# Optimization experiments

Hardware: AMD Instinct MI355X
Metric: run time of the kernel (lower is better)

Reference implementation:

```python
import jax, jax.numpy as jnp
import numpy as np

N_NODES = 10000
N_EDGES = 320000
H = 256
L = 3
EPS = 1e-5


def _mlp2(x, w1, b1, w2, b2):
    # Linear -> ReLU -> Linear
    return jax.nn.relu(x @ w1 + b1) @ w2 + b2


def _layer_norm(x, g, b):
    mu = jnp.mean(x, axis=-1, keepdims=True)
    var = jnp.var(x, axis=-1, keepdims=True)
    return (x - mu) * jax.lax.rsqrt(var + EPS) * g + b


def setup_inputs() -> dict:
    key = jax.random.key(0)
    ks = jax.random.split(key, 24)
    s = 0.02
    inp = {
        "node_features": jax.random.normal(ks[0], (N_NODES, H), dtype=jnp.float32),
        "edge_index": jax.random.randint(ks[1], (2, N_EDGES), 0, N_NODES, dtype=jnp.int64),
        # node encoder (Linear 256->256, ReLU, Linear 256->256)
        "ne_w1": jax.random.normal(ks[2], (H, H), dtype=jnp.float32) * s,
        "ne_b1": jnp.zeros((H,), jnp.float32),
        "ne_w2": jax.random.normal(ks[3], (H, H), dtype=jnp.float32) * s,
        "ne_b2": jnp.zeros((H,), jnp.float32),
        # per-layer message MLP (2H->H, ReLU, H->H), stacked over L layers
        "msg_w1": jax.random.normal(ks[4], (L, 2 * H, H), dtype=jnp.float32) * s,
        "msg_b1": jnp.zeros((L, H), jnp.float32),
        "msg_w2": jax.random.normal(ks[5], (L, H, H), dtype=jnp.float32) * s,
        "msg_b2": jnp.zeros((L, H), jnp.float32),
        # per-layer update MLP (2H->H, ReLU, H->H)
        "upd_w1": jax.random.normal(ks[6], (L, 2 * H, H), dtype=jnp.float32) * s,
        "upd_b1": jnp.zeros((L, H), jnp.float32),
        "upd_w2": jax.random.normal(ks[7], (L, H, H), dtype=jnp.float32) * s,
        "upd_b2": jnp.zeros((L, H), jnp.float32),
        # per-layer LayerNorm
        "ln_g": jnp.ones((L, H), jnp.float32),
        "ln_b": jnp.zeros((L, H), jnp.float32),
        # readout MLP
        "ro_w1": jax.random.normal(ks[8], (H, H), dtype=jnp.float32) * s,
        "ro_b1": jnp.zeros((H,), jnp.float32),
        "ro_w2": jax.random.normal(ks[9], (H, H), dtype=jnp.float32) * s,
        "ro_b2": jnp.zeros((H,), jnp.float32),
    }
    return inp


def reference(node_features, edge_index, ne_w1, ne_b1, ne_w2, ne_b2,
              msg_w1, msg_b1, msg_w2, msg_b2,
              upd_w1, upd_b1, upd_w2, upd_b2,
              ln_g, ln_b, ro_w1, ro_b1, ro_w2, ro_b2):
    n_nodes = node_features.shape[0]
    src, dst = edge_index[0], edge_index[1]

    # node encoder
    x = _mlp2(node_features, ne_w1, ne_b1, ne_w2, ne_b2)  # [N, H]

    # message passing layers (edge_attr is unused in the original layer)
    for l in range(L):
        cat_e = jnp.concatenate([x[src], x[dst]], axis=-1)          # [E, 2H]
        messages = _mlp2(cat_e, msg_w1[l], msg_b1[l], msg_w2[l], msg_b2[l])  # [E, H]
        aggregated = jax.ops.segment_sum(messages, dst, num_segments=n_nodes)  # [N, H]
        cat_n = jnp.concatenate([x, aggregated], axis=-1)           # [N, 2H]
        updated = _mlp2(cat_n, upd_w1[l], upd_b1[l], upd_w2[l], upd_b2[l])
        x = _layer_norm(x + updated, ln_g[l], ln_b[l])

    # mean readout
    g = jnp.mean(x, axis=0)  # [H]
    return _mlp2(g, ro_w1, ro_b1, ro_w2, ro_b2)  # [H]
```

## Files before the change

### kernel.cpp

```cpp
#include <hip/hip_runtime.h>

#define NN 10000
#define NE 320000
#define HD 256
#define NL 3

typedef unsigned short ushort_t;
typedef __attribute__((ext_vector_type(8))) short bf16x8;
typedef __attribute__((ext_vector_type(4))) float f32x4;

#define MFMA __builtin_amdgcn_mfma_f32_16x16x32_bf16

#define WAITV(N) asm volatile("s_waitcnt vmcnt(" #N ")" ::: "memory")
#define SCHEDPIN() __builtin_amdgcn_sched_barrier(0)
#define LGKMBAR() do { asm volatile("s_waitcnt lgkmcnt(0)" ::: "memory"); \
                       __builtin_amdgcn_s_barrier(); __builtin_amdgcn_sched_barrier(0); } while (0)

__device__ __forceinline__ unsigned short f2bf(float x) {
    unsigned u = __float_as_uint(x);
    unsigned rounding = 0x7FFFu + ((u >> 16) & 1u);
    return (unsigned short)((u + rounding) >> 16);
}
__device__ __forceinline__ float bf2f(unsigned short u) {
    return __uint_as_float(((unsigned)u) << 16);
}
__device__ __forceinline__ bf16x8 cvt8(float4 lo, float4 hi) {
    bf16x8 r;
    r[0] = (short)f2bf(lo.x); r[1] = (short)f2bf(lo.y);
    r[2] = (short)f2bf(lo.z); r[3] = (short)f2bf(lo.w);
    r[4] = (short)f2bf(hi.x); r[5] = (short)f2bf(hi.y);
    r[6] = (short)f2bf(hi.z); r[7] = (short)f2bf(hi.w);
    return r;
}
__device__ __forceinline__ void dma16(const void* g, void* l) {
    __builtin_amdgcn_global_load_lds(
        (const __attribute__((address_space(1))) unsigned int*)g,
        (__attribute__((address_space(3))) unsigned int*)l, 16, 0, 0);
}


__global__ void hist_deg(const int* __restrict__ dst, int* __restrict__ deg, int E) {
    int e = blockIdx.x * blockDim.x + threadIdx.x;
    if (e < E) atomicAdd(&deg[dst[e]], 1);
}

__global__ __launch_bounds__(1024) void scan_csr(const int* __restrict__ deg,
                                                 int* __restrict__ row_start,
                                                 int* __restrict__ cursor,
                                                 float* __restrict__ degf,
                                                 float* __restrict__ gsum, int n) {
    __shared__ int wsum[16];
    __shared__ int carry_s;
    int tid = threadIdx.x, lane = tid & 63, wid = tid >> 6;
    if (tid < HD) gsum[tid] = 0.f;
    if (tid == 0) carry_s = 0;
    __syncthreads();
    for (int base = 0; base < n; base += 1024) {
        int i = base + tid;
        int v = (i < n) ? deg[i] : 0;
        int s = v;
        #pragma unroll
        for (int off = 1; off < 64; off <<= 1) {
            int t = __shfl_up(s, off);
            if (lane >= off) s += t;
        }
        if (lane == 63) wsum[wid] = s;
        __syncthreads();
        if (wid == 0 && lane < 16) {
            int ws = wsum[lane];
            #pragma unroll
            for (int off = 1; off < 16; off <<= 1) {
                int t = __shfl_up(ws, off);
                if (lane >= off) ws += t;
            }
            wsum[lane] = ws;
        }
        __syncthreads();
        int carry = carry_s;
        int wpre = (wid > 0) ? wsum[wid - 1] : 0;
        int incl = carry + wpre + s;
        int excl = incl - v;
        if (i < n) { row_start[i] = excl; cursor[i] = excl; degf[i] = (float)v; }
        __syncthreads();
        if (tid == 1023) carry_s = incl;
        __syncthreads();
    }
    if (tid == 0) row_start[n] = carry_s;
}

__global__ void scatter_src(const int* __restrict__ src, const int* __restrict__ dst,
                            int* __restrict__ cursor, int* __restrict__ src_sorted, int E) {
    int e = blockIdx.x * blockDim.x + threadIdx.x;
    if (e < E) {
        int pos = atomicAdd(&cursor[dst[e]], 1);
        src_sorted[pos] = src[e];
    }
}


struct TDesc { const float* src; ushort_t* dst; int transpose; };
struct TArgs { TDesc d[20]; };

__global__ __launch_bounds__(256) void conv_t(TArgs args) {
    __shared__ ushort_t tile[64][65];
    const float* src = args.d[blockIdx.y].src;
    ushort_t* dst = args.d[blockIdx.y].dst;
    int tr = args.d[blockIdx.y].transpose;
    int t = blockIdx.x;
    int r0 = (t >> 2) * 64, c0 = (t & 3) * 64;
    int tid = threadIdx.x;
    int rr = tid >> 4, cc4 = (tid & 15) * 4;
    if (!tr) {
        #pragma unroll
        for (int i = 0; i < 4; ++i) {
            int r = r0 + rr + i * 16;
            float4 v = *(const float4*)(src + (size_t)r * HD + c0 + cc4);
            ushort4 o = { f2bf(v.x), f2bf(v.y), f2bf(v.z), f2bf(v.w) };
            *(ushort4*)(dst + (size_t)r * HD + c0 + cc4) = o;
        }
        return;
    }
    #pragma unroll
    for (int i = 0; i < 4; ++i) {
        int r = rr + i * 16;
        float4 v = *(const float4*)(src + (size_t)(r0 + r) * HD + c0 + cc4);
        tile[cc4 + 0][r] = f2bf(v.x);
        tile[cc4 + 1][r] = f2bf(v.y);
        tile[cc4 + 2][r] = f2bf(v.z);
        tile[cc4 + 3][r] = f2bf(v.w);
    }
    __syncthreads();
    #pragma unroll
    for (int i = 0; i < 4; ++i) {
        int c = rr + i * 16;
        ushort4 o = { tile[c][cc4], tile[c][cc4 + 1], tile[c][cc4 + 2], tile[c][cc4 + 3] };
        *(ushort4*)(dst + (size_t)(c0 + c) * HD + r0 + cc4) = o;
    }
}

__global__ __launch_bounds__(256) void bias_compose(const float* __restrict__ mb2,
                                                    const float* __restrict__ uw1,
                                                    float* __restrict__ out) {
    int l = blockIdx.x, c = threadIdx.x;
    const float* b2l = mb2 + (size_t)l * HD;
    const float* u1b = uw1 + (size_t)l * 2 * HD * HD + (size_t)HD * HD;
    float s = 0.f;
    for (int k = 0; k < HD; ++k) s += b2l[k] * u1b[(size_t)k * HD + c];
    out[(size_t)l * HD + c] = s;
}

__global__ __launch_bounds__(256) void gemm_w2u(
    const ushort_t* __restrict__ Abase, const ushort_t* __restrict__ Btbase,
    ushort_t* __restrict__ outBase)
{
    const ushort_t* A  = Abase  + (size_t)blockIdx.z * HD * HD;
    const ushort_t* Bt = Btbase + (size_t)blockIdx.z * HD * HD;
    ushort_t* outB     = outBase + (size_t)blockIdx.z * HD * HD;
    int tid = threadIdx.x;
    int wid = tid >> 6, lane = tid & 63;
    int wm = wid >> 1, wn = wid & 1;
    int row0 = blockIdx.x * 64 + wm * 32;
    int col0 = blockIdx.y * 64 + wn * 32;
    int lm = lane & 15, lk = (lane >> 4) * 8;
    f32x4 acc[2][2] = {};
    const ushort_t* a0p = A + (size_t)(row0 + lm) * HD + lk;
    const ushort_t* a1p = A + (size_t)(row0 + 16 + lm) * HD + lk;
    const ushort_t* b0p = Bt + (size_t)(col0 + lm) * HD + lk;
    const ushort_t* b1p = Bt + (size_t)(col0 + 16 + lm) * HD + lk;
    #pragma unroll
    for (int k0 = 0; k0 < HD; k0 += 32) {
        bf16x8 a0 = *(const bf16x8*)(a0p + k0);
        bf16x8 a1 = *(const bf16x8*)(a1p + k0);
        bf16x8 b0 = *(const bf16x8*)(b0p + k0);
        bf16x8 b1 = *(const bf16x8*)(b1p + k0);
        acc[0][0] = MFMA(a0, b0, acc[0][0], 0, 0, 0);
        acc[0][1] = MFMA(a0, b1, acc[0][1], 0, 0, 0);
        acc[1][0] = MFMA(a1, b0, acc[1][0], 0, 0, 0);
        acc[1][1] = MFMA(a1, b1, acc[1][1], 0, 0, 0);
    }
    int orow = (lane >> 4) * 4;
    #pragma unroll
    for (int mi = 0; mi < 2; ++mi)
        #pragma unroll
        for (int r = 0; r < 4; ++r) {
            int row = row0 + mi * 16 + orow + r;
            #pragma unroll
            for (int ni = 0; ni < 2; ++ni) {
                int col = col0 + ni * 16 + lm;
                outB[(size_t)row * HD + col] = f2bf(acc[mi][ni][r]);
            }
        }
}

__device__ __forceinline__ int swz(int row, int byte_in_row) {
    return row * 512 + (byte_in_row ^ ((row & 7) << 4));
}


__global__ __launch_bounds__(512, 4) void enc_pq(
    const float* __restrict__ A, const ushort_t* __restrict__ B1t,
    const ushort_t* __restrict__ B2t,
    const float* __restrict__ b1, const float* __restrict__ b2,
    const ushort_t* __restrict__ Pw1t, const ushort_t* __restrict__ Pw1b,
    const float* __restrict__ pqb1,
    float* __restrict__ xF, ushort_t* __restrict__ xB,
    ushort_t* __restrict__ P, float* __restrict__ Q, int M)
{
    __shared__ char wlds[8][2][2][2048];
    __shared__ char hid[16 * 512];
    int tid = threadIdx.x;
    int w = tid >> 6, lane = tid & 63;
    int lm = lane & 15, q = lane >> 4;
    int row0 = blockIdx.x * 16;
    int col0 = w * 32;
    int cA = col0 + lm, cB = col0 + 16 + lm;

    auto stageW = [&](const ushort_t* Mt, int k0, int p, int m) {
        #pragma unroll
        for (int i = 0; i < 2; ++i) {
            int col = col0 + 16 * i + (lane >> 2);
            int qs = (lane & 3) ^ (col & 3) ^ ((col >> 2) & 3);
            dma16((const char*)Mt + (size_t)col * 512 + k0 * 2 + qs * 16,
                  wlds[w][p][m] + i * 1024);
        }
    };
    auto readB = [&](int p, int m, int ni) -> bf16x8 {
        int col = col0 + 16 * ni + lm;
        int q2 = q ^ (col & 3) ^ ((col >> 2) & 3);
        return *(const bf16x8*)(wlds[w][p][m] + ni * 1024 + lm * 64 + q2 * 16);
    };

    float b1v[2] = { b1[cA], b1[cB] };
    float b2v[2] = { b2[cA], b2[cB] };
    float pqv[2] = { pqb1[cA], pqb1[cB] };

    const float* ap = A + (size_t)(row0 + lm) * HD + q * 8;
    float4 alo[2], ahi[2];
    #pragma unroll
    for (int s = 0; s < 2; ++s) {
        stageW(B1t, s * 32, s, 0);
        alo[s] = *(const float4*)(ap + s * 32);
        ahi[s] = *(const float4*)(ap + s * 32 + 4);
        SCHEDPIN();
    }

    f32x4 acc[2] = {};
    #pragma unroll
    for (int j = 0; j < 8; ++j) {
        int p = j & 1;
        if (j < 7) { WAITV(4); } else { WAITV(0); }
        bf16x8 a = cvt8(alo[p], ahi[p]);
        acc[0] = MFMA(a, readB(p, 0, 0), acc[0], 0, 0, 0);
        acc[1] = MFMA(a, readB(p, 0, 1), acc[1], 0, 0, 0);
        SCHEDPIN();
        if (j < 6) {
            stageW(B1t, (j + 2) * 32, p, 0);
            alo[p] = *(const float4*)(ap + (j + 2) * 32);
            ahi[p] = *(const float4*)(ap + (j + 2) * 32 + 4);
            SCHEDPIN();
        }
    }

    #pragma unroll
    for (int s = 0; s < 2; ++s) { stageW(B2t, s * 32, s, 0); SCHEDPIN(); }
    #pragma unroll
    for (int ni = 0; ni < 2; ++ni) {
        int col = col0 + 16 * ni + lm;
        #pragma unroll
        for (int r = 0; r < 4; ++r) {
            int row = 4 * q + r;
            float v = fmaxf(acc[ni][r] + b1v[ni], 0.f);
            *(ushort_t*)(hid + swz(row, col * 2)) = f2bf(v);
        }
    }
    LGKMBAR();

    f32x4 acc2[2] = {};
    #pragma unroll
    for (int j = 0; j < 8; ++j) {
        int p = j & 1;
        if (j < 7) { WAITV(2); } else { WAITV(0); }
        int bk = (j * 32 + q * 8) * 2;
        bf16x8 a = *(const bf16x8*)(hid + swz(lm, bk));
        acc2[0] = MFMA(a, readB(p, 0, 0), acc2[0], 0, 0, 0);
        acc2[1] = MFMA(a, readB(p, 0, 1), acc2[1], 0, 0, 0);
        SCHEDPIN();
        if (j < 6) { stageW(B2t, (j + 2) * 32, p, 0); SCHEDPIN(); }
    }

    #pragma unroll
    for (int s = 0; s < 2; ++s) {
        stageW(Pw1t, s * 32, s, 0);
        stageW(Pw1b, s * 32, s, 1);
        SCHEDPIN();
    }
    LGKMBAR();
    #pragma unroll
    for (int ni = 0; ni < 2; ++ni) {
        int col = col0 + 16 * ni + lm;
        #pragma unroll
        for (int r = 0; r < 4; ++r) {
            int row = 4 * q + r;
            int grow = row0 + row;
            float v = acc2[ni][r] + b2v[ni];
            *(ushort_t*)(hid + swz(row, col * 2)) = f2bf(v);
            xF[(size_t)grow * HD + col] = v;
            xB[(size_t)grow * HD + col] = f2bf(v);
        }
    }
    LGKMBAR();

    f32x4 aP[2] = {}, aQ[2] = {};
    #pragma unroll
    for (int j = 0; j < 8; ++j) {
        int p = j & 1;
        if (j < 7) { WAITV(4); } else { WAITV(0); }
        int bk = (j * 32 + q * 8) * 2;
        bf16x8 a = *(const bf16x8*)(hid + swz(lm, bk));
        #pragma unroll
        for (int ni = 0; ni < 2; ++ni) {
            aP[ni] = MFMA(a, readB(p, 0, ni), aP[ni], 0, 0, 0);
            aQ[ni] = MFMA(a, readB(p, 1, ni), aQ[ni], 0, 0, 0);
        }
        SCHEDPIN();
        if (j < 6) {
            stageW(Pw1t, (j + 2) * 32, p, 0);
            stageW(Pw1b, (j + 2) * 32, p, 1);
            SCHEDPIN();
        }
    }
    #pragma unroll
    for (int r = 0; r < 4; ++r) {
        int grow = row0 + 4 * q + r;
        #pragma unroll
        for (int ni = 0; ni < 2; ++ni) {
            int col = col0 + 16 * ni + lm;
            P[(size_t)grow * HD + col] = f2bf(aP[ni][r]);
            Q[(size_t)grow * HD + col] = aQ[ni][r] + pqv[ni];
        }
    }
}


__global__ __launch_bounds__(256) void edge_agg(
    const ushort_t* __restrict__ Pb, const float* __restrict__ Qf,
    const int* __restrict__ row_start, const int* __restrict__ srcs,
    ushort_t* __restrict__ Haggb)
{
    int node = blockIdx.x * 4 + (threadIdx.x >> 6);
    int lane = threadIdx.x & 63;
    int c4 = lane * 4;
    float4 qb = *(const float4*)(Qf + (size_t)node * HD + c4);
    float4 acc = {0.f, 0.f, 0.f, 0.f};
    int j = row_start[node], e = row_start[node + 1];
    for (; j + 8 <= e; j += 8) {
        ushort4 p[8];
        #pragma unroll
        for (int u = 0; u < 8; ++u) {
            int s = srcs[j + u];
            p[u] = *(const ushort4*)(Pb + (size_t)s * HD + c4);
        }
        #pragma unroll
        for (int u = 0; u < 8; ++u) {
            acc.x += fmaxf(bf2f(p[u].x) + qb.x, 0.f);
            acc.y += fmaxf(bf2f(p[u].y) + qb.y, 0.f);
            acc.z += fmaxf(bf2f(p[u].z) + qb.z, 0.f);
            acc.w += fmaxf(bf2f(p[u].w) + qb.w, 0.f);
        }
    }
    for (; j < e; ++j) {
        int s0 = srcs[j];
        ushort4 p0 = *(const ushort4*)(Pb + (size_t)s0 * HD + c4);
        acc.x += fmaxf(bf2f(p0.x) + qb.x, 0.f);
        acc.y += fmaxf(bf2f(p0.y) + qb.y, 0.f);
        acc.z += fmaxf(bf2f(p0.z) + qb.z, 0.f);
        acc.w += fmaxf(bf2f(p0.w) + qb.w, 0.f);
    }
    ushort4 o = { f2bf(acc.x), f2bf(acc.y), f2bf(acc.z), f2bf(acc.w) };
    *(ushort4*)(Haggb + (size_t)node * HD + c4) = o;
}


__global__ __launch_bounds__(512, 4) void upd_ln(
    const ushort_t* __restrict__ xb, const ushort_t* __restrict__ Hb,
    const ushort_t* __restrict__ B1t, const ushort_t* __restrict__ B2t,
    const ushort_t* __restrict__ B3t,
    const float* __restrict__ degf,
    const float* __restrict__ b1, const float* __restrict__ bias2,
    const float* __restrict__ b3,
    const float* __restrict__ g, const float* __restrict__ bb,
    const ushort_t* __restrict__ Pw1t, const ushort_t* __restrict__ Pw1b,
    const float* __restrict__ pqb1,
    float* __restrict__ gsum,
    float* __restrict__ xF, ushort_t* __restrict__ xB,
    ushort_t* __restrict__ P, float* __restrict__ Q, int M)
{
    __shared__ char wlds[8][2][2][2048];
    __shared__ char hid[16 * 512];
    __shared__ float sS[8][16], sQ[8][16], muv[16], ivv[16];

    int tid = threadIdx.x;
    int w = tid >> 6, lane = tid & 63;
    int lm = lane & 15, q = lane >> 4;
    int row0 = blockIdx.x * 16;
    int col0 = w * 32;
    int cA = col0 + lm, cB = col0 + 16 + lm;

    auto stageW = [&](const ushort_t* Mt, int k0, int p, int m) {
        #pragma unroll
        for (int i = 0; i < 2; ++i) {
            int col = col0 + 16 * i + (lane >> 2);
            int qs = (lane & 3) ^ (col & 3) ^ ((col >> 2) & 3);
            dma16((const char*)Mt + (size_t)col * 512 + k0 * 2 + qs * 16,
                  wlds[w][p][m] + i * 1024);
        }
    };
    auto readB = [&](int p, int m, int ni) -> bf16x8 {
        int col = col0 + 16 * ni + lm;
        int q2 = q ^ (col & 3) ^ ((col >> 2) & 3);
        return *(const bf16x8*)(wlds[w][p][m] + ni * 1024 + lm * 64 + q2 * 16);
    };

    float b1v[2] = { b1[cA], b1[cB] };
    float bzv[2] = { bias2[cA], bias2[cB] };
    float b3v[2] = { b3[cA], b3[cB] };
    float gv[2]  = { g[cA],  g[cB]  };
    float bbv[2] = { bb[cA], bb[cB] };
    float pqv[2] = { Pw1t ? pqb1[cA] : 0.f, Pw1t ? pqb1[cB] : 0.f };
    float dgv[4], res[2][4];
    #pragma unroll
    for (int r = 0; r < 4; ++r) {
        int row = 4 * q + r;
        dgv[r] = degf[row0 + row];
        res[0][r] = xF[(size_t)(row0 + row) * HD + cA];
        res[1][r] = xF[(size_t)(row0 + row) * HD + cB];
    }

    const ushort_t* xp = xb + (size_t)(row0 + lm) * HD + q * 8;
    const ushort_t* hp = Hb + (size_t)(row0 + lm) * HD + q * 8;
    bf16x8 ax[2], ah[2];
    #pragma unroll
    for (int s = 0; s < 2; ++s) {
        stageW(B1t, s * 32, s, 0);
        stageW(B2t, s * 32, s, 1);
        ax[s] = *(const bf16x8*)(xp + s * 32);
        ah[s] = *(const bf16x8*)(hp + s * 32);
        SCHEDPIN();
    }

    f32x4 acc[2] = {};
    #pragma unroll
    for (int j = 0; j < 8; ++j) {
        int p = j & 1;
        if (j < 7) { WAITV(6); } else { WAITV(0); }
        #pragma unroll
        for (int ni = 0; ni < 2; ++ni) {
            acc[ni] = MFMA(ax[p], readB(p, 0, ni), acc[ni], 0, 0, 0);
            acc[ni] = MFMA(ah[p], readB(p, 1, ni), acc[ni], 0, 0, 0);
        }
        SCHEDPIN();
        if (j < 6) {
            stageW(B1t, (j + 2) * 32, p, 0);
            stageW(B2t, (j + 2) * 32, p, 1);
            ax[p] = *(const bf16x8*)(xp + (j + 2) * 32);
            ah[p] = *(const bf16x8*)(hp + (j + 2) * 32);
            SCHEDPIN();
        }
    }

    #pragma unroll
    for (int s = 0; s < 2; ++s) { stageW(B3t, s * 32, s, 0); SCHEDPIN(); }
    #pragma unroll
    for (int r = 0; r < 4; ++r) {
        int row = 4 * q + r;
        #pragma unroll
        for (int ni = 0; ni < 2; ++ni) {
            int col = col0 + 16 * ni + lm;
            float v = fmaxf(acc[ni][r] + b1v[ni] + dgv[r] * bzv[ni], 0.f);
            *(ushort_t*)(hid + swz(row, col * 2)) = f2bf(v);
        }
    }
    LGKMBAR();

    f32x4 acc2[2] = {};
    #pragma unroll
    for (int j = 0; j < 8; ++j) {
        int p = j & 1;
        if (j < 7) { WAITV(2); } else { WAITV(0); }
        int bk = (j * 32 + q * 8) * 2;
        bf16x8 a = *(const bf16x8*)(hid + swz(lm, bk));
        acc2[0] = MFMA(a, readB(p, 0, 0), acc2[0], 0, 0, 0);
        acc2[1] = MFMA(a, readB(p, 0, 1), acc2[1], 0, 0, 0);
        SCHEDPIN();
        if (j < 6) { stageW(B3t, (j + 2) * 32, p, 0); SCHEDPIN(); }
    }

    if (Pw1t) {
        #pragma unroll
        for (int s = 0; s < 2; ++s) {
            stageW(Pw1t, s * 32, s, 0);
            stageW(Pw1b, s * 32, s, 1);
            SCHEDPIN();
        }
    }
    #pragma unroll
    for (int r = 0; r < 4; ++r) {
        float s = 0.f, qq = 0.f;
        #pragma unroll
        for (int ni = 0; ni < 2; ++ni) {
            float v = acc2[ni][r] + b3v[ni] + res[ni][r];
            acc2[ni][r] = v;
            s += v; qq += v * v;
        }
        #pragma unroll
        for (int off = 1; off < 16; off <<= 1) {
            s += __shfl_xor(s, off);
            qq += __shfl_xor(qq, off);
        }
        if (lm == 0) {
            int row = 4 * q + r;
            sS[w][row] = s; sQ[w][row] = qq;
        }
    }
    LGKMBAR();
    if (tid < 16) {
        float s = 0.f, qq = 0.f;
        #pragma unroll
        for (int i = 0; i < 8; ++i) { s += sS[i][tid]; qq += sQ[i][tid]; }
        float mu = s * (1.0f / HD);
        float var = qq * (1.0f / HD) - mu * mu;
        muv[tid] = mu;
        ivv[tid] = rsqrtf(var + 1e-5f);
    }
    LGKMBAR();
    float csum[2] = {0.f, 0.f};
    #pragma unroll
    for (int r = 0; r < 4; ++r) {
        int row = 4 * q + r;
        int grow = row0 + row;
        float mu = muv[row], iv = ivv[row];
        #pragma unroll
        for (int ni = 0; ni < 2; ++ni) {
            int col = col0 + 16 * ni + lm;
            float o = (acc2[ni][r] - mu) * iv * gv[ni] + bbv[ni];
            *(ushort_t*)(hid + swz(row, col * 2)) = f2bf(o);
            xF[(size_t)grow * HD + col] = o;
            xB[(size_t)grow * HD + col] = f2bf(o);
            csum[ni] += o;
        }
    }
    if (gsum) {
        #pragma unroll
        for (int ni = 0; ni < 2; ++ni) {
            float s = csum[ni];
            s += __shfl_xor(s, 16);
            s += __shfl_xor(s, 32);
            if (q == 0) atomicAdd(&gsum[col0 + 16 * ni + lm], s);
        }
    }

    if (Pw1t) {
        LGKMBAR();
        f32x4 aP[2] = {}, aQ[2] = {};
        #pragma unroll
        for (int j = 0; j < 8; ++j) {
            int p = j & 1;
            if (j < 7) { WAITV(4); } else { WAITV(0); }
            int bk = (j * 32 + q * 8) * 2;
            bf16x8 a = *(const bf16x8*)(hid + swz(lm, bk));
            #pragma unroll
            for (int ni = 0; ni < 2; ++ni) {
                aP[ni] = MFMA(a, readB(p, 0, ni), aP[ni], 0, 0, 0);
                aQ[ni] = MFMA(a, readB(p, 1, ni), aQ[ni], 0, 0, 0);
            }
            SCHEDPIN();
            if (j < 6) {
                stageW(Pw1t, (j + 2) * 32, p, 0);
                stageW(Pw1b, (j + 2) * 32, p, 1);
                SCHEDPIN();
            }
        }
        #pragma unroll
        for (int r = 0; r < 4; ++r) {
            int grow = row0 + 4 * q + r;
            #pragma unroll
            for (int ni = 0; ni < 2; ++ni) {
                int col = col0 + 16 * ni + lm;
                P[(size_t)grow * HD + col] = f2bf(aP[ni][r]);
                Q[(size_t)grow * HD + col] = aQ[ni][r] + pqv[ni];
            }
        }
    }
}


__global__ __launch_bounds__(256) void readout_mlp(
    const float* __restrict__ gsum,
    const float* __restrict__ w1, const float* __restrict__ b1,
    const float* __restrict__ w2, const float* __restrict__ b2,
    float* __restrict__ out, float invn)
{
    __shared__ float gl[HD], h1[HD];
    int c = threadIdx.x;
    gl[c] = gsum[c] * invn;
    __syncthreads();
    float a = b1[c];
    for (int k = 0; k < HD; ++k) a += gl[k] * w1[k * HD + c];
    h1[c] = fmaxf(a, 0.f);
    __syncthreads();
    float o = b2[c];
    for (int k = 0; k < HD; ++k) o += h1[k] * w2[k * HD + c];
    out[c] = o;
}


extern "C" void kernel_launch(void* const* d_in, const int* in_sizes, int n_in,
                              void* d_out, int out_size, void* d_ws, size_t ws_size,
                              hipStream_t stream) {
    const float* nf    = (const float*)d_in[0];
    const int*   ei    = (const int*)d_in[1];
    const float* ne_w1 = (const float*)d_in[2];
    const float* ne_b1 = (const float*)d_in[3];
    const float* ne_w2 = (const float*)d_in[4];
    const float* ne_b2 = (const float*)d_in[5];
    const float* mw1   = (const float*)d_in[6];
    const float* mb1   = (const float*)d_in[7];
    const float* mw2   = (const float*)d_in[8];
    const float* mb2   = (const float*)d_in[9];
    const float* uw1   = (const float*)d_in[10];
    const float* ub1   = (const float*)d_in[11];
    const float* uw2   = (const float*)d_in[12];
    const float* ub2   = (const float*)d_in[13];
    const float* lng   = (const float*)d_in[14];
    const float* lnb   = (const float*)d_in[15];
    const float* rw1   = (const float*)d_in[16];
    const float* rb1   = (const float*)d_in[17];
    const float* rw2   = (const float*)d_in[18];
    const float* rb2   = (const float*)d_in[19];

    const int* e_src = ei;
    const int* e_dst = ei + NE;

    char* w = (char*)d_ws;
    size_t off = 0;
    auto alloc = [&](size_t bytes) -> void* {
        void* p = w + off;
        off = (off + bytes + 255) & ~(size_t)255;
        return p;
    };
    const size_t NF32 = (size_t)NN * HD * sizeof(float);
    const size_t NF16 = (size_t)NN * HD * sizeof(ushort_t);
    const size_t WM16 = (size_t)HD * HD * sizeof(ushort_t);

    float* x    = (float*)alloc(NF32);
    float* Qf   = (float*)alloc(NF32);
    float* gsum = (float*)alloc(HD * sizeof(float));
    float* degf = (float*)alloc(NN * sizeof(float));
    float* b2u1 = (float*)alloc(NL * HD * sizeof(float));

    ushort_t* xb    = (ushort_t*)alloc(NF16);
    ushort_t* Pb    = (ushort_t*)alloc(NF16);
    ushort_t* Haggb = (ushort_t*)alloc(NF16);
    ushort_t* neT1  = (ushort_t*)alloc(WM16);
    ushort_t* neT2  = (ushort_t*)alloc(WM16);
    ushort_t* w1tT  = (ushort_t*)alloc(NL * WM16);
    ushort_t* w1bT  = (ushort_t*)alloc(NL * WM16);
    ushort_t* u1tT  = (ushort_t*)alloc(NL * WM16);
    ushort_t* u1bT  = (ushort_t*)alloc(NL * WM16);
    ushort_t* u2T   = (ushort_t*)alloc(NL * WM16);
    ushort_t* w2uT  = (ushort_t*)alloc(NL * WM16);
    ushort_t* w2rmb = (ushort_t*)alloc(NL * WM16);

    int* deg       = (int*)alloc(NN * sizeof(int));
    int* row_start = (int*)alloc((NN + 1) * sizeof(int));
    int* cursor    = (int*)alloc(NN * sizeof(int));
    int* srcs      = (int*)alloc(NE * sizeof(int));

    hipMemsetAsync(deg, 0, NN * sizeof(int), stream);

    hist_deg<<<(NE + 255) / 256, 256, 0, stream>>>(e_dst, deg, NE);
    scan_csr<<<1, 1024, 0, stream>>>(deg, row_start, cursor, degf, gsum, NN);
    scatter_src<<<(NE + 255) / 256, 256, 0, stream>>>(e_src, e_dst, cursor, srcs, NE);

    TArgs ta;
    ta.d[0] = { ne_w1, neT1, 1 };
    ta.d[1] = { ne_w2, neT2, 1 };
    for (int l = 0; l < NL; ++l) {
        const float* w1l = mw1 + (size_t)l * 2 * HD * HD;
        const float* u1l = uw1 + (size_t)l * 2 * HD * HD;
        ta.d[2 + l]  = { w1l,                       w1tT + (size_t)l * HD * HD, 1 };
        ta.d[5 + l]  = { w1l + (size_t)HD * HD,     w1bT + (size_t)l * HD * HD, 1 };
        ta.d[8 + l]  = { u1l,                       u1tT + (size_t)l * HD * HD, 1 };
        ta.d[11 + l] = { u1l + (size_t)HD * HD,     u1bT + (size_t)l * HD * HD, 1 };
        ta.d[14 + l] = { uw2 + (size_t)l * HD * HD, u2T + (size_t)l * HD * HD, 1 };
        ta.d[17 + l] = { mw2 + (size_t)l * HD * HD, w2rmb + (size_t)l * HD * HD, 0 };
    }
    conv_t<<<dim3(16, 20), 256, 0, stream>>>(ta);
    bias_compose<<<NL, 256, 0, stream>>>(mb2, uw1, b2u1);
    gemm_w2u<<<dim3(4, 4, NL), 256, 0, stream>>>(u1bT, w2rmb, w2uT);

    enc_pq<<<NN / 16, 512, 0, stream>>>(nf, neT1, neT2, ne_b1, ne_b2,
                                        w1tT, w1bT, mb1, x, xb, Pb, Qf, NN);

    for (int l = 0; l < NL; ++l) {
        edge_agg<<<NN / 4, 256, 0, stream>>>(Pb, Qf, row_start, srcs, Haggb);
        int nl = l + 1;
        const ushort_t* pw1t = (nl < NL) ? w1tT + (size_t)nl * HD * HD : nullptr;
        const ushort_t* pw1b = (nl < NL) ? w1bT + (size_t)nl * HD * HD : nullptr;
        const float*    pqb1 = (nl < NL) ? mb1 + (size_t)nl * HD : nullptr;
        float* gs = (l == NL - 1) ? gsum : nullptr;
        upd_ln<<<NN / 16, 512, 0, stream>>>(
            xb, Haggb, u1tT + (size_t)l * HD * HD, w2uT + (size_t)l * HD * HD,
            u2T + (size_t)l * HD * HD, degf,
            ub1 + (size_t)l * HD, b2u1 + (size_t)l * HD, ub2 + (size_t)l * HD,
            lng + (size_t)l * HD, lnb + (size_t)l * HD,
            pw1t, pw1b, pqb1, gs, x, xb, Pb, Qf, NN);
    }

    readout_mlp<<<1, 256, 0, stream>>>(gsum, rw1, rb1, rw2, rb2, (float*)d_out, 1.0f / NN);
}
```

Measured before the change: 306.5 us.

## Pre-tile weights and activations into k-slab swizzled layouts for contiguous DMA

Weights are now converted into a k-slab-major, pre-swizzled bf16 layout, so each wave's global-to-LDS DMA reads one contiguous 1KB chunk instead of 16-byte pieces strided across rows. The node features are cast to bf16 in a separate tiled kernel, which removes the fp32 loads and per-element conversion from the encoder. Activations (xb, Hagg) are written in a matching 16-row tiled layout so the A-operand loads are contiguous. The cost is one extra cast kernel and extra index arithmetic on the scattered output stores.

```diff
diff --git a/kernel.cpp b/kernel.cpp
--- a/kernel.cpp
+++ b/kernel.cpp
@@ -24,14 +24,7 @@
 __device__ __forceinline__ float bf2f(unsigned short u) {
     return __uint_as_float(((unsigned)u) << 16);
 }
-__device__ __forceinline__ bf16x8 cvt8(float4 lo, float4 hi) {
-    bf16x8 r;
-    r[0] = (short)f2bf(lo.x); r[1] = (short)f2bf(lo.y);
-    r[2] = (short)f2bf(lo.z); r[3] = (short)f2bf(lo.w);
-    r[4] = (short)f2bf(hi.x); r[5] = (short)f2bf(hi.y);
-    r[6] = (short)f2bf(hi.z); r[7] = (short)f2bf(hi.w);
-    return r;
-}
+__device__ __forceinline__ int sw2(int col) { return (col & 3) ^ ((col >> 2) & 3); }
 __device__ __forceinline__ void dma16(const void* g, void* l) {
     __builtin_amdgcn_global_load_lds(
         (const __attribute__((address_space(1))) unsigned int*)g,
@@ -98,19 +91,19 @@
 }
 
 
-struct TDesc { const float* src; ushort_t* dst; int transpose; };
+struct TDesc { const float* src; ushort_t* dst; int mode; };
 struct TArgs { TDesc d[20]; };
 
 __global__ __launch_bounds__(256) void conv_t(TArgs args) {
     __shared__ ushort_t tile[64][65];
     const float* src = args.d[blockIdx.y].src;
     ushort_t* dst = args.d[blockIdx.y].dst;
-    int tr = args.d[blockIdx.y].transpose;
+    int mode = args.d[blockIdx.y].mode;
     int t = blockIdx.x;
     int r0 = (t >> 2) * 64, c0 = (t & 3) * 64;
     int tid = threadIdx.x;
     int rr = tid >> 4, cc4 = (tid & 15) * 4;
-    if (!tr) {
+    if (mode == 0) {
         #pragma unroll
         for (int i = 0; i < 4; ++i) {
             int r = r0 + rr + i * 16;
@@ -134,7 +127,29 @@
     for (int i = 0; i < 4; ++i) {
         int c = rr + i * 16;
         ushort4 o = { tile[c][cc4], tile[c][cc4 + 1], tile[c][cc4 + 2], tile[c][cc4 + 3] };
-        *(ushort4*)(dst + (size_t)(c0 + c) * HD + r0 + cc4) = o;
+        if (mode == 1) {
+            *(ushort4*)(dst + (size_t)(c0 + c) * HD + r0 + cc4) = o;
+        } else {
+            int col = c0 + c;
+            int k = r0 + cc4;
+            int s = k >> 5, qv = (k >> 3) & 3;
+            int slot = qv ^ sw2(col);
+            *(ushort4*)(dst + (size_t)s * 8192 + col * 32 + slot * 8 + (k & 7)) = o;
+        }
+    }
+}
+
+__global__ __launch_bounds__(256) void cast_nf_tiled(const float* __restrict__ src,
+                                                     ushort_t* __restrict__ dst) {
+    int blk = blockIdx.x;
+    int row = threadIdx.x >> 4, g = threadIdx.x & 15;
+    const float* sp = src + ((size_t)blk * 16 + row) * HD + g * 16;
+    ushort_t* dp = dst + (size_t)blk * 4096 + (g >> 1) * 512 + row * 32 + (g & 1) * 16;
+    #pragma unroll
+    for (int j = 0; j < 4; ++j) {
+        float4 v = *(const float4*)(sp + j * 4);
+        ushort4 o = { f2bf(v.x), f2bf(v.y), f2bf(v.z), f2bf(v.w) };
+        *(ushort4*)(dp + j * 4) = o;
     }
 }
 
@@ -187,7 +202,9 @@
             #pragma unroll
             for (int ni = 0; ni < 2; ++ni) {
                 int col = col0 + ni * 16 + lm;
-                outB[(size_t)row * HD + col] = f2bf(acc[mi][ni][r]);
+                int s = col >> 5, qv = (col >> 3) & 3;
+                int slot = qv ^ sw2(row);
+                outB[(size_t)s * 8192 + row * 32 + slot * 8 + (col & 7)] = f2bf(acc[mi][ni][r]);
             }
         }
 }
@@ -198,7 +215,7 @@
 
 
 __global__ __launch_bounds__(512, 4) void enc_pq(
-    const float* __restrict__ A, const ushort_t* __restrict__ B1t,
+    const ushort_t* __restrict__ Anf, const ushort_t* __restrict__ B1t,
     const ushort_t* __restrict__ B2t,
     const float* __restrict__ b1, const float* __restrict__ b2,
     const ushort_t* __restrict__ Pw1t, const ushort_t* __restrict__ Pw1b,
@@ -215,18 +232,15 @@
     int col0 = w * 32;
     int cA = col0 + lm, cB = col0 + 16 + lm;
 
-    auto stageW = [&](const ushort_t* Mt, int k0, int p, int m) {
-        #pragma unroll
-        for (int i = 0; i < 2; ++i) {
-            int col = col0 + 16 * i + (lane >> 2);
-            int qs = (lane & 3) ^ (col & 3) ^ ((col >> 2) & 3);
-            dma16((const char*)Mt + (size_t)col * 512 + k0 * 2 + qs * 16,
+    auto stageW = [&](const ushort_t* Wt, int s, int p, int m) {
+        #pragma unroll
+        for (int i = 0; i < 2; ++i)
+            dma16((const char*)Wt + (size_t)s * 16384 + (col0 + 16 * i) * 64 + lane * 16,
                   wlds[w][p][m] + i * 1024);
-        }
     };
     auto readB = [&](int p, int m, int ni) -> bf16x8 {
         int col = col0 + 16 * ni + lm;
-        int q2 = q ^ (col & 3) ^ ((col >> 2) & 3);
+        int q2 = q ^ sw2(col);
         return *(const bf16x8*)(wlds[w][p][m] + ni * 1024 + lm * 64 + q2 * 16);
     };
 
@@ -234,13 +248,12 @@
     float b2v[2] = { b2[cA], b2[cB] };
     float pqv[2] = { pqb1[cA], pqb1[cB] };
 
-    const float* ap = A + (size_t)(row0 + lm) * HD + q * 8;
-    float4 alo[2], ahi[2];
+    const ushort_t* ap = Anf + (size_t)blockIdx.x * 4096 + lm * 32 + q * 8;
+    bf16x8 ax[2];
     #pragma unroll
     for (int s = 0; s < 2; ++s) {
-        stageW(B1t, s * 32, s, 0);
-        alo[s] = *(const float4*)(ap + s * 32);
-        ahi[s] = *(const float4*)(ap + s * 32 + 4);
+        stageW(B1t, s, s, 0);
+        ax[s] = *(const bf16x8*)(ap + s * 512);
         SCHEDPIN();
     }
 
@@ -248,21 +261,19 @@
     #pragma unroll
     for (int j = 0; j < 8; ++j) {
         int p = j & 1;
-        if (j < 7) { WAITV(4); } else { WAITV(0); }
-        bf16x8 a = cvt8(alo[p], ahi[p]);
-        acc[0] = MFMA(a, readB(p, 0, 0), acc[0], 0, 0, 0);
-        acc[1] = MFMA(a, readB(p, 0, 1), acc[1], 0, 0, 0);
+        if (j < 7) { WAITV(3); } else { WAITV(0); }
+        acc[0] = MFMA(ax[p], readB(p, 0, 0), acc[0], 0, 0, 0);
+        acc[1] = MFMA(ax[p], readB(p, 0, 1), acc[1], 0, 0, 0);
         SCHEDPIN();
         if (j < 6) {
-            stageW(B1t, (j + 2) * 32, p, 0);
-            alo[p] = *(const float4*)(ap + (j + 2) * 32);
-            ahi[p] = *(const float4*)(ap + (j + 2) * 32 + 4);
+            stageW(B1t, j + 2, p, 0);
+            ax[p] = *(const bf16x8*)(ap + (j + 2) * 512);
             SCHEDPIN();
         }
     }
 
     #pragma unroll
-    for (int s = 0; s < 2; ++s) { stageW(B2t, s * 32, s, 0); SCHEDPIN(); }
+    for (int s = 0; s < 2; ++s) { stageW(B2t, s, s, 0); SCHEDPIN(); }
     #pragma unroll
     for (int ni = 0; ni < 2; ++ni) {
         int col = col0 + 16 * ni + lm;
@@ -285,16 +296,17 @@
         acc2[0] = MFMA(a, readB(p, 0, 0), acc2[0], 0, 0, 0);
         acc2[1] = MFMA(a, readB(p, 0, 1), acc2[1], 0, 0, 0);
         SCHEDPIN();
-        if (j < 6) { stageW(B2t, (j + 2) * 32, p, 0); SCHEDPIN(); }
+        if (j < 6) { stageW(B2t, j + 2, p, 0); SCHEDPIN(); }
     }
 
     #pragma unroll
     for (int s = 0; s < 2; ++s) {
-        stageW(Pw1t, s * 32, s, 0);
-        stageW(Pw1b, s * 32, s, 1);
+        stageW(Pw1t, s, s, 0);
+        stageW(Pw1b, s, s, 1);
         SCHEDPIN();
     }
     LGKMBAR();
+    int tbase = blockIdx.x * 4096 + w * 512;
     #pragma unroll
     for (int ni = 0; ni < 2; ++ni) {
         int col = col0 + 16 * ni + lm;
@@ -305,7 +317,7 @@
             float v = acc2[ni][r] + b2v[ni];
             *(ushort_t*)(hid + swz(row, col * 2)) = f2bf(v);
             xF[(size_t)grow * HD + col] = v;
-            xB[(size_t)grow * HD + col] = f2bf(v);
+            xB[tbase + row * 32 + 16 * ni + lm] = f2bf(v);
         }
     }
     LGKMBAR();
@@ -324,8 +336,8 @@
         }
         SCHEDPIN();
         if (j < 6) {
-            stageW(Pw1t, (j + 2) * 32, p, 0);
-            stageW(Pw1b, (j + 2) * 32, p, 1);
+            stageW(Pw1t, j + 2, p, 0);
+            stageW(Pw1b, j + 2, p, 1);
             SCHEDPIN();
         }
     }
@@ -345,7 +357,7 @@
 __global__ __launch_bounds__(256) void edge_agg(
     const ushort_t* __restrict__ Pb, const float* __restrict__ Qf,
     const int* __restrict__ row_start, const int* __restrict__ srcs,
-    ushort_t* __restrict__ Haggb)
+    ushort_t* __restrict__ HaggT)
 {
     int node = blockIdx.x * 4 + (threadIdx.x >> 6);
     int lane = threadIdx.x & 63;
@@ -377,7 +389,8 @@
         acc.w += fmaxf(bf2f(p0.w) + qb.w, 0.f);
     }
     ushort4 o = { f2bf(acc.x), f2bf(acc.y), f2bf(acc.z), f2bf(acc.w) };
-    *(ushort4*)(Haggb + (size_t)node * HD + c4) = o;
+    int tidx = (node >> 4) * 4096 + (c4 >> 5) * 512 + (node & 15) * 32 + (c4 & 31);
+    *(ushort4*)(HaggT + tidx) = o;
 }
 
 
@@ -406,20 +419,29 @@
     int col0 = w * 32;
     int cA = col0 + lm, cB = col0 + 16 + lm;
 
-    auto stageW = [&](const ushort_t* Mt, int k0, int p, int m) {
-        #pragma unroll
-        for (int i = 0; i < 2; ++i) {
-            int col = col0 + 16 * i + (lane >> 2);
-            int qs = (lane & 3) ^ (col & 3) ^ ((col >> 2) & 3);
-            dma16((const char*)Mt + (size_t)col * 512 + k0 * 2 + qs * 16,
+    auto stageW = [&](const ushort_t* Wt, int s, int p, int m) {
+        #pragma unroll
+        for (int i = 0; i < 2; ++i)
+            dma16((const char*)Wt + (size_t)s * 16384 + (col0 + 16 * i) * 64 + lane * 16,
                   wlds[w][p][m] + i * 1024);
-        }
     };
     auto readB = [&](int p, int m, int ni) -> bf16x8 {
         int col = col0 + 16 * ni + lm;
-        int q2 = q ^ (col & 3) ^ ((col >> 2) & 3);
+        int q2 = q ^ sw2(col);
         return *(const bf16x8*)(wlds[w][p][m] + ni * 1024 + lm * 64 + q2 * 16);
     };
+
+    const ushort_t* xp = xb + (size_t)blockIdx.x * 4096 + lm * 32 + q * 8;
+    const ushort_t* hp = Hb + (size_t)blockIdx.x * 4096 + lm * 32 + q * 8;
+    bf16x8 ax[2], ah[2];
+    #pragma unroll
+    for (int s = 0; s < 2; ++s) {
+        stageW(B1t, s, s, 0);
+        stageW(B2t, s, s, 1);
+        ax[s] = *(const bf16x8*)(xp + s * 512);
+        ah[s] = *(const bf16x8*)(hp + s * 512);
+        SCHEDPIN();
+    }
 
     float b1v[2] = { b1[cA], b1[cB] };
     float bzv[2] = { bias2[cA], bias2[cB] };
@@ -436,18 +458,6 @@
         res[1][r] = xF[(size_t)(row0 + row) * HD + cB];
     }
 
-    const ushort_t* xp = xb + (size_t)(row0 + lm) * HD + q * 8;
-    const ushort_t* hp = Hb + (size_t)(row0 + lm) * HD + q * 8;
-    bf16x8 ax[2], ah[2];
-    #pragma unroll
-    for (int s = 0; s < 2; ++s) {
-        stageW(B1t, s * 32, s, 0);
-        stageW(B2t, s * 32, s, 1);
-        ax[s] = *(const bf16x8*)(xp + s * 32);
-        ah[s] = *(const bf16x8*)(hp + s * 32);
-        SCHEDPIN();
-    }
-
     f32x4 acc[2] = {};
     #pragma unroll
     for (int j = 0; j < 8; ++j) {
@@ -460,16 +470,16 @@
         }
         SCHEDPIN();
         if (j < 6) {
-            stageW(B1t, (j + 2) * 32, p, 0);
-            stageW(B2t, (j + 2) * 32, p, 1);
-            ax[p] = *(const bf16x8*)(xp + (j + 2) * 32);
-            ah[p] = *(const bf16x8*)(hp + (j + 2) * 32);
+            stageW(B1t, j + 2, p, 0);
+            stageW(B2t, j + 2, p, 1);
+            ax[p] = *(const bf16x8*)(xp + (j + 2) * 512);
+            ah[p] = *(const bf16x8*)(hp + (j + 2) * 512);
             SCHEDPIN();
         }
     }
 
     #pragma unroll
-    for (int s = 0; s < 2; ++s) { stageW(B3t, s * 32, s, 0); SCHEDPIN(); }
+    for (int s = 0; s < 2; ++s) { stageW(B3t, s, s, 0); SCHEDPIN(); }
     #pragma unroll
     for (int r = 0; r < 4; ++r) {
         int row = 4 * q + r;
@@ -492,14 +502,14 @@
         acc2[0] = MFMA(a, readB(p, 0, 0), acc2[0], 0, 0, 0);
         acc2[1] = MFMA(a, readB(p, 0, 1), acc2[1], 0, 0, 0);
         SCHEDPIN();
-        if (j < 6) { stageW(B3t, (j + 2) * 32, p, 0); SCHEDPIN(); }
+        if (j < 6) { stageW(B3t, j + 2, p, 0); SCHEDPIN(); }
     }
 
     if (Pw1t) {
         #pragma unroll
         for (int s = 0; s < 2; ++s) {
-            stageW(Pw1t, s * 32, s, 0);
-            stageW(Pw1b, s * 32, s, 1);
+            stageW(Pw1t, s, s, 0);
+            stageW(Pw1b, s, s, 1);
             SCHEDPIN();
         }
     }
@@ -534,6 +544,7 @@
     }
     LGKMBAR();
     float csum[2] = {0.f, 0.f};
+    int tbase = blockIdx.x * 4096 + w * 512;
     #pragma unroll
     for (int r = 0; r < 4; ++r) {
         int row = 4 * q + r;
@@ -545,7 +556,7 @@
             float o = (acc2[ni][r] - mu) * iv * gv[ni] + bbv[ni];
             *(ushort_t*)(hid + swz(row, col * 2)) = f2bf(o);
             xF[(size_t)grow * HD + col] = o;
-            xB[(size_t)grow * HD + col] = f2bf(o);
+            xB[tbase + row * 32 + 16 * ni + lm] = f2bf(o);
             csum[ni] += o;
         }
     }
@@ -575,8 +586,8 @@
             }
             SCHEDPIN();
             if (j < 6) {
-                stageW(Pw1t, (j + 2) * 32, p, 0);
-                stageW(Pw1b, (j + 2) * 32, p, 1);
+                stageW(Pw1t, j + 2, p, 0);
+                stageW(Pw1b, j + 2, p, 1);
                 SCHEDPIN();
             }
         }
@@ -658,6 +669,7 @@
     float* degf = (float*)alloc(NN * sizeof(float));
     float* b2u1 = (float*)alloc(NL * HD * sizeof(float));
 
+    ushort_t* nfT   = (ushort_t*)alloc(NF16);
     ushort_t* xb    = (ushort_t*)alloc(NF16);
     ushort_t* Pb    = (ushort_t*)alloc(NF16);
     ushort_t* Haggb = (ushort_t*)alloc(NF16);
@@ -683,23 +695,24 @@
     scatter_src<<<(NE + 255) / 256, 256, 0, stream>>>(e_src, e_dst, cursor, srcs, NE);
 
     TArgs ta;
-    ta.d[0] = { ne_w1, neT1, 1 };
-    ta.d[1] = { ne_w2, neT2, 1 };
+    ta.d[0] = { ne_w1, neT1, 2 };
+    ta.d[1] = { ne_w2, neT2, 2 };
     for (int l = 0; l < NL; ++l) {
         const float* w1l = mw1 + (size_t)l * 2 * HD * HD;
         const float* u1l = uw1 + (size_t)l * 2 * HD * HD;
-        ta.d[2 + l]  = { w1l,                       w1tT + (size_t)l * HD * HD, 1 };
-        ta.d[5 + l]  = { w1l + (size_t)HD * HD,     w1bT + (size_t)l * HD * HD, 1 };
-        ta.d[8 + l]  = { u1l,                       u1tT + (size_t)l * HD * HD, 1 };
+        ta.d[2 + l]  = { w1l,                       w1tT + (size_t)l * HD * HD, 2 };
+        ta.d[5 + l]  = { w1l + (size_t)HD * HD,     w1bT + (size_t)l * HD * HD, 2 };
+        ta.d[8 + l]  = { u1l,                       u1tT + (size_t)l * HD * HD, 2 };
         ta.d[11 + l] = { u1l + (size_t)HD * HD,     u1bT + (size_t)l * HD * HD, 1 };
-        ta.d[14 + l] = { uw2 + (size_t)l * HD * HD, u2T + (size_t)l * HD * HD, 1 };
+        ta.d[14 + l] = { uw2 + (size_t)l * HD * HD, u2T + (size_t)l * HD * HD, 2 };
         ta.d[17 + l] = { mw2 + (size_t)l * HD * HD, w2rmb + (size_t)l * HD * HD, 0 };
     }
     conv_t<<<dim3(16, 20), 256, 0, stream>>>(ta);
+    cast_nf_tiled<<<NN / 16, 256, 0, stream>>>(nf, nfT);
     bias_compose<<<NL, 256, 0, stream>>>(mb2, uw1, b2u1);
     gemm_w2u<<<dim3(4, 4, NL), 256, 0, stream>>>(u1bT, w2rmb, w2uT);
 
-    enc_pq<<<NN / 16, 512, 0, stream>>>(nf, neT1, neT2, ne_b1, ne_b2,
+    enc_pq<<<NN / 16, 512, 0, stream>>>(nfT, neT1, neT2, ne_b1, ne_b2,
                                         w1tT, w1bT, mb1, x, xb, Pb, Qf, NN);
 
     for (int l = 0; l < NL; ++l) {
```

Result: faster. 285.3 us (-6.9%).
